# Kernel optimization log

Hardware: AMD Instinct MI355X
Metric: run time of the kernel (lower is better)

## Reference

```python
import jax, jax.numpy as jnp
import numpy as np

D_HEAD = 64
KV_GROUPS = 3
KSIZE = 7


def _win_idx(L, ksize):
    # NATTEN neighborhood: window centered at i, shifted to stay in-bounds.
    start = jnp.clip(jnp.arange(L) - ksize // 2, 0, L - ksize)  # [L]
    return start[:, None] + jnp.arange(ksize)[None, :]          # [L, k]


def _natten2d(q, k, v, ksize):
    # q,k,v: [n, nh, H, W, e]; q pre-scaled.
    H, W = q.shape[2], q.shape[3]
    ih = _win_idx(H, ksize)  # [H, k]
    iw = _win_idx(W, ksize)  # [W, k]
    # gather per-query key/value windows: [n, nh, H, W, k, k, e]
    kg = k[:, :, ih[:, None, :, None], iw[None, :, None, :], :]
    vg = v[:, :, ih[:, None, :, None], iw[None, :, None, :], :]
    logits = jnp.einsum('nhije,nhijabe->nhijab', q, kg)  # [n,nh,H,W,k,k]
    n_, nh = logits.shape[:2]
    a = jax.nn.softmax(logits.reshape(n_, nh, H, W, ksize * ksize), axis=-1)
    a = a.reshape(logits.shape)
    return jnp.einsum('nhijab,nhijabe->nhije', a, vg)  # [n,nh,H,W,e]


def _to_heads(p, nh, e):
    n, h, w, _ = p.shape
    return p.reshape(n, h, w, nh, e).transpose(0, 3, 1, 2, 4)  # [n,nh,h,w,e]


def setup_inputs() -> dict:
    key = jax.random.key(0)
    k1, k2, k3 = jax.random.split(key, 3)
    x = jax.random.normal(k1, (2, 32, 32, 768), dtype=jnp.float32)
    w_qkv = jax.random.normal(k2, (1280, 768), dtype=jnp.float32) * 0.02
    w_out = jax.random.normal(k3, (768, 768), dtype=jnp.float32) * 0.02
    return {"x": x, "w_qkv": w_qkv, "w_out": w_out}


def reference(x, w_qkv, w_out):
    n, H, W, d_model = x.shape
    q_heads = d_model // D_HEAD
    kv_heads = q_heads // KV_GROUPS
    qkv = x @ w_qkv.T  # [n,H,W,1280]
    q, k, v = jnp.split(
        qkv, [q_heads * D_HEAD, (q_heads + kv_heads) * D_HEAD], axis=-1)
    q = _to_heads(q, q_heads, D_HEAD)
    k = jnp.tile(_to_heads(k, kv_heads, D_HEAD), (1, KV_GROUPS, 1, 1, 1))
    v = jnp.tile(_to_heads(v, kv_heads, D_HEAD), (1, KV_GROUPS, 1, 1, 1))
    q = q / (D_HEAD ** 0.5)
    o = _natten2d(q, k, v, KSIZE)           # [n,nh,H,W,e]
    o = o.transpose(0, 2, 3, 1, 4).reshape(n, H, W, d_model)
    return o @ w_out.T
```

## Files before the change

### kernel.cpp

```cpp
#include <hip/hip_runtime.h>
#include <hip/hip_bf16.h>


typedef __attribute__((ext_vector_type(8))) __bf16 bf16x8;
typedef __attribute__((ext_vector_type(4))) float floatx4;
typedef unsigned short u16;

__device__ inline u16 f2bf(float f) {
    union { float f; unsigned u; } v; v.f = f;
    return (u16)((v.u + 0x7fff + ((v.u >> 16) & 1)) >> 16);
}

__device__ inline void gl_lds16(const void* g, void* l) {
    __builtin_amdgcn_global_load_lds(
        (const __attribute__((address_space(1))) void*)g,
        (__attribute__((address_space(3))) void*)l, 16, 0, 0);
}

__global__ __launch_bounds__(256) void convert_kernel(
    const float* __restrict__ x, const float* __restrict__ w1,
    const float* __restrict__ w2, u16* __restrict__ xb,
    u16* __restrict__ w1b, u16* __restrict__ w2b)
{
    int t = blockIdx.x * blockDim.x + threadIdx.x;
    const float* s; u16* d;
    if (t < 393216)      { s = x;  d = xb; }
    else if (t < 638976) { s = w1; d = w1b; t -= 393216; }
    else                 { s = w2; d = w2b; t -= 638976; }
    float4 v = ((const float4*)s)[t];
    ushort4 o;
    o.x = f2bf(v.x); o.y = f2bf(v.y); o.z = f2bf(v.z); o.w = f2bf(v.w);
    ((ushort4*)d)[t] = o;
}

template<int MODE>
__global__ __launch_bounds__(256) void gemm_nt(
    const u16* __restrict__ A, const u16* __restrict__ B,
    float* __restrict__ C, u16* __restrict__ Cb, u16* __restrict__ vT,
    int M, int N, int K)
{
    __shared__ __align__(16) u16 As[128 * 32];
    __shared__ __align__(16) u16 Bs[64 * 32];
    const int tid = threadIdx.x;
    const int lane = tid & 63;
    const int wave = tid >> 6;
    const int bm = blockIdx.y * 128;
    const int bn = blockIdx.x * 64;
    const int qr = (wave >> 1) * 64;
    const int qc = (wave & 1) * 32;

    floatx4 acc[4][2] = {};

    const int srA0 = wave * 32 + (lane >> 2);
    const int srA1 = srA0 + 16;
    const int srB  = wave * 16 + (lane >> 2);
    const int skel = (lane & 3) * 8;
    const u16* Ap0 = A + (size_t)(bm + srA0) * K + skel;
    const u16* Ap1 = A + (size_t)(bm + srA1) * K + skel;
    const u16* Bp  = B + (size_t)(bn + srB)  * K + skel;
    u16* AsC0 = &As[(wave * 2 + 0) * 512];
    u16* AsC1 = &As[(wave * 2 + 1) * 512];
    u16* BsC  = &Bs[wave * 512];

    const int fr = lane & 15;
    const int fk = (lane >> 4) * 8;

    for (int k0 = 0; k0 < K; k0 += 32) {
        gl_lds16(Ap0 + k0, AsC0);
        gl_lds16(Ap1 + k0, AsC1);
        gl_lds16(Bp  + k0, BsC);
        __syncthreads();
        bf16x8 af[4], bf[2];
        #pragma unroll
        for (int i = 0; i < 4; i++)
            af[i] = *(const bf16x8*)&As[(qr + i * 16 + fr) * 32 + fk];
        #pragma unroll
        for (int j = 0; j < 2; j++)
            bf[j] = *(const bf16x8*)&Bs[(qc + j * 16 + fr) * 32 + fk];
        #pragma unroll
        for (int i = 0; i < 4; i++)
            #pragma unroll
            for (int j = 0; j < 2; j++)
                acc[i][j] = __builtin_amdgcn_mfma_f32_16x16x32_bf16(
                    af[i], bf[j], acc[i][j], 0, 0, 0);
        __syncthreads();
    }

    const int cr = (lane >> 4) * 4;
    const int cc = lane & 15;
    #pragma unroll
    for (int i = 0; i < 4; i++) {
        #pragma unroll
        for (int j = 0; j < 2; j++) {
            const int row0 = bm + qr + i * 16 + cr;
            const int col  = bn + qc + j * 16 + cc;
            if (MODE == 0) {
                #pragma unroll
                for (int r = 0; r < 4; r++)
                    C[(size_t)(row0 + r) * N + col] = acc[i][j][r];
            } else {
                if (col < 1024) {
                    #pragma unroll
                    for (int r = 0; r < 4; r++)
                        Cb[(size_t)(row0 + r) * 1024 + col] = f2bf(acc[i][j][r]);
                } else {
                    ushort4 w;
                    w.x = f2bf(acc[i][j][0]); w.y = f2bf(acc[i][j][1]);
                    w.z = f2bf(acc[i][j][2]); w.w = f2bf(acc[i][j][3]);
                    *(ushort4*)&vT[(size_t)(col - 1024) * 2048 + row0] = w;
                }
            }
        }
    }
}

__global__ __launch_bounds__(256) void natten_mfma(
    const u16* __restrict__ qkv, const u16* __restrict__ vT,
    u16* __restrict__ o)
{
    __shared__ __align__(16) u16 Ks[224 * 72];
    __shared__ __align__(16) u16 Vs[64 * 224];
    __shared__ __align__(16) u16 Pw[4 * 512];
    const int h  = blockIdx.x;
    const int tb = blockIdx.y;
    const int g  = h & 3;
    const int batch = tb >> 4;
    const int ti = ((tb >> 2) & 3) * 8;
    const int tj = (tb & 3) * 8;
    const int wu_i = min(max(ti - 3, 0), 18);
    const int wu_j = min(max(tj - 3, 0), 18);
    const int tid = threadIdx.x, lane = tid & 63, wave = tid >> 6;
    const int pixbase = batch << 10;

    for (int c = tid; c < 1792; c += 256) {
        int n = c >> 3, seg = (c & 7) * 8;
        int a = n >> 4, b = min(n & 15, 13);
        int pix = pixbase + (wu_i + a) * 32 + wu_j + b;
        *(uint4*)&Ks[n * 72 + seg] =
            *(const uint4*)&qkv[(size_t)pix * 1024 + 768 + g * 64 + seg];
    }
    for (int c = tid; c < 14336; c += 256) {
        int d = c / 224, n = c % 224;
        int a = n >> 4, b = n & 15;
        u16 val = 0;
        if (b < 14) {
            int pix = pixbase + (wu_i + a) * 32 + wu_j + b;
            val = vT[(size_t)(g * 64 + d) * 2048 + pix];
        }
        Vs[d * 224 + n] = val;
    }
    __syncthreads();

    const int fr = lane & 15;
    const int fk = (lane >> 4) * 8;

    bf16x8 aq0, aq1;
    {
        int qq = wave * 16 + fr;
        int pixq = pixbase + (ti + (qq >> 3)) * 32 + tj + (qq & 7);
        const u16* qp = &qkv[(size_t)pixq * 1024 + h * 64];
        aq0 = *(const bf16x8*)(qp + fk);
        aq1 = *(const bf16x8*)(qp + 32 + fk);
    }

    bool colok[4]; int tlo[4], thi[4];
    #pragma unroll
    for (int r = 0; r < 4; r++) {
        int qq = wave * 16 + (lane >> 4) * 4 + r;
        int qi = ti + (qq >> 3), qj = tj + (qq & 7);
        int si = min(max(qi - 3, 0), 25);
        int sj = min(max(qj - 3, 0), 25);
        colok[r] = (fr < 14) && (wu_j + fr >= sj) && (wu_j + fr <= sj + 6);
        tlo[r] = si - wu_i; thi[r] = tlo[r] + 6;
    }

    float s[14][4];
    float mx[4] = {-1e30f, -1e30f, -1e30f, -1e30f};
    #pragma unroll
    for (int t = 0; t < 14; t++) {
        bf16x8 bk0 = *(const bf16x8*)&Ks[(t * 16 + fr) * 72 + fk];
        bf16x8 bk1 = *(const bf16x8*)&Ks[(t * 16 + fr) * 72 + 32 + fk];
        floatx4 a4 = {};
        a4 = __builtin_amdgcn_mfma_f32_16x16x32_bf16(aq0, bk0, a4, 0, 0, 0);
        a4 = __builtin_amdgcn_mfma_f32_16x16x32_bf16(aq1, bk1, a4, 0, 0, 0);
        #pragma unroll
        for (int r = 0; r < 4; r++) {
            bool v = colok[r] && (t >= tlo[r]) && (t <= thi[r]);
            s[t][r] = v ? a4[r] * 0.125f : -1e30f;
            mx[r] = fmaxf(mx[r], s[t][r]);
        }
    }
    #pragma unroll
    for (int r = 0; r < 4; r++) {
        mx[r] = fmaxf(mx[r], __shfl_xor(mx[r], 1));
        mx[r] = fmaxf(mx[r], __shfl_xor(mx[r], 2));
        mx[r] = fmaxf(mx[r], __shfl_xor(mx[r], 4));
        mx[r] = fmaxf(mx[r], __shfl_xor(mx[r], 8));
    }
    float l[4] = {0.f, 0.f, 0.f, 0.f};
    #pragma unroll
    for (int t = 0; t < 14; t++)
        #pragma unroll
        for (int r = 0; r < 4; r++) {
            float p = __expf(s[t][r] - mx[r]);
            s[t][r] = p; l[r] += p;
        }
    #pragma unroll
    for (int r = 0; r < 4; r++) {
        l[r] += __shfl_xor(l[r], 1);
        l[r] += __shfl_xor(l[r], 2);
        l[r] += __shfl_xor(l[r], 4);
        l[r] += __shfl_xor(l[r], 8);
    }
    float rinv[4];
    #pragma unroll
    for (int r = 0; r < 4; r++) rinv[r] = 1.0f / l[r];

    u16* pw = &Pw[wave * 512];
    floatx4 oacc[4] = {};
    #pragma unroll
    for (int kc = 0; kc < 7; kc++) {
        #pragma unroll
        for (int tt = 0; tt < 2; tt++) {
            int t = kc * 2 + tt;
            #pragma unroll
            for (int r = 0; r < 4; r++)
                pw[((lane >> 4) * 4 + r) * 32 + tt * 16 + fr] =
                    f2bf(s[t][r] * rinv[r]);
        }
        bf16x8 bp = *(const bf16x8*)&pw[fr * 32 + fk];
        #pragma unroll
        for (int u = 0; u < 4; u++) {
            bf16x8 av = *(const bf16x8*)&Vs[(u * 16 + fr) * 224 + kc * 32 + fk];
            oacc[u] = __builtin_amdgcn_mfma_f32_16x16x32_bf16(av, bp, oacc[u], 0, 0, 0);
        }
    }

    {
        int qq = wave * 16 + fr;
        int pixq = pixbase + (ti + (qq >> 3)) * 32 + tj + (qq & 7);
        u16* op = &o[(size_t)pixq * 768 + h * 64];
        #pragma unroll
        for (int u = 0; u < 4; u++) {
            ushort4 w;
            w.x = f2bf(oacc[u][0]); w.y = f2bf(oacc[u][1]);
            w.z = f2bf(oacc[u][2]); w.w = f2bf(oacc[u][3]);
            *(ushort4*)(op + u * 16 + (lane >> 4) * 4) = w;
        }
    }
}

extern "C" void kernel_launch(void* const* d_in, const int* in_sizes, int n_in,
                              void* d_out, int out_size, void* d_ws, size_t ws_size,
                              hipStream_t stream)
{
    const float* x     = (const float*)d_in[0];
    const float* w_qkv = (const float*)d_in[1];
    const float* w_out = (const float*)d_in[2];
    float* out = (float*)d_out;

    char* ws = (char*)d_ws;
    u16* qkvb = (u16*)ws; ws += (size_t)2048 * 1024 * 2;
    u16* vTb  = (u16*)ws; ws += (size_t)256 * 2048 * 2 + 64;
    u16* xb   = (u16*)ws; ws += (size_t)2048 * 768 * 2;
    u16* w1b  = (u16*)ws; ws += (size_t)1280 * 768 * 2;
    u16* w2b  = (u16*)ws; ws += (size_t)768 * 768 * 2;
    u16* ob   = (u16*)ws;

    convert_kernel<<<dim3(3072), dim3(256), 0, stream>>>(x, w_qkv, w_out, xb, w1b, w2b);

    gemm_nt<1><<<dim3(1280 / 64, 2048 / 128), dim3(256), 0, stream>>>(
        xb, w1b, nullptr, qkvb, vTb, 2048, 1280, 768);

    natten_mfma<<<dim3(12, 32), dim3(256), 0, stream>>>(qkvb, vTb, ob);

    gemm_nt<0><<<dim3(768 / 64, 2048 / 128), dim3(256), 0, stream>>>(
        ob, w2b, out, nullptr, nullptr, 2048, 768, 768);
}
```

Measured before the change: 123.1 us.

## Use 64x64 GEMM tiles with 128-deep K stages and restructure V tile load

The GEMM tile shrinks from 128x64 to 64x64, doubling the grid size. Each stage now loads 128 K-elements via eight direct-to-LDS loads per wave, so there are fewer barriers per K and more MFMAs per sync. The NATTEN V-transpose staging loop replaces per-element division and modulo with a wave-per-16-rows layout using precomputed offsets. The aim is better occupancy on small GEMMs and fewer loop-overhead and index costs, at the price of less operand reuse per tile and larger LDS use.

```diff
diff --git a/kernel.cpp b/kernel.cpp
--- a/kernel.cpp
+++ b/kernel.cpp
@@ -39,61 +39,63 @@
     float* __restrict__ C, u16* __restrict__ Cb, u16* __restrict__ vT,
     int M, int N, int K)
 {
-    __shared__ __align__(16) u16 As[128 * 32];
-    __shared__ __align__(16) u16 Bs[64 * 32];
+    __shared__ __align__(16) u16 As[4 * 64 * 32];
+    __shared__ __align__(16) u16 Bs[4 * 64 * 32];
     const int tid = threadIdx.x;
     const int lane = tid & 63;
     const int wave = tid >> 6;
-    const int bm = blockIdx.y * 128;
+    const int bm = blockIdx.y * 64;
     const int bn = blockIdx.x * 64;
-    const int qr = (wave >> 1) * 64;
+    const int qr = (wave >> 1) * 32;
     const int qc = (wave & 1) * 32;
 
-    floatx4 acc[4][2] = {};
-
-    const int srA0 = wave * 32 + (lane >> 2);
-    const int srA1 = srA0 + 16;
-    const int srB  = wave * 16 + (lane >> 2);
-    const int skel = (lane & 3) * 8;
-    const u16* Ap0 = A + (size_t)(bm + srA0) * K + skel;
-    const u16* Ap1 = A + (size_t)(bm + srA1) * K + skel;
-    const u16* Bp  = B + (size_t)(bn + srB)  * K + skel;
-    u16* AsC0 = &As[(wave * 2 + 0) * 512];
-    u16* AsC1 = &As[(wave * 2 + 1) * 512];
-    u16* BsC  = &Bs[wave * 512];
+    floatx4 acc[2][2] = {};
+
+    const u16* Xsrc = (wave < 2) ? A : B;
+    const int   bx  = (wave < 2) ? bm : bn;
+    u16* Xlds       = (wave < 2) ? As : Bs;
+    const int half  = wave & 1;
+    const int l2 = lane >> 2;
+    const int l3 = (lane & 3) * 8;
+    const u16* gptr[8];
+    u16* lptr[8];
+    #pragma unroll
+    for (int cc = 0; cc < 8; cc++) {
+        int c = half * 8 + cc, kc = c & 3, rg = c >> 2;
+        gptr[cc] = Xsrc + (size_t)(bx + rg * 16 + l2) * K + kc * 32 + l3;
+        lptr[cc] = Xlds + kc * 2048 + rg * 512;
+    }
 
     const int fr = lane & 15;
     const int fk = (lane >> 4) * 8;
 
-    for (int k0 = 0; k0 < K; k0 += 32) {
-        gl_lds16(Ap0 + k0, AsC0);
-        gl_lds16(Ap1 + k0, AsC1);
-        gl_lds16(Bp  + k0, BsC);
+    for (int k0 = 0; k0 < K; k0 += 128) {
+        #pragma unroll
+        for (int cc = 0; cc < 8; cc++)
+            gl_lds16(gptr[cc] + k0, lptr[cc]);
         __syncthreads();
-        bf16x8 af[4], bf[2];
-        #pragma unroll
-        for (int i = 0; i < 4; i++)
-            af[i] = *(const bf16x8*)&As[(qr + i * 16 + fr) * 32 + fk];
-        #pragma unroll
-        for (int j = 0; j < 2; j++)
-            bf[j] = *(const bf16x8*)&Bs[(qc + j * 16 + fr) * 32 + fk];
-        #pragma unroll
-        for (int i = 0; i < 4; i++)
-            #pragma unroll
-            for (int j = 0; j < 2; j++)
-                acc[i][j] = __builtin_amdgcn_mfma_f32_16x16x32_bf16(
-                    af[i], bf[j], acc[i][j], 0, 0, 0);
+        #pragma unroll
+        for (int kc = 0; kc < 4; kc++) {
+            bf16x8 af0 = *(const bf16x8*)&As[kc * 2048 + (qr +      fr) * 32 + fk];
+            bf16x8 af1 = *(const bf16x8*)&As[kc * 2048 + (qr + 16 + fr) * 32 + fk];
+            bf16x8 bf0 = *(const bf16x8*)&Bs[kc * 2048 + (qc +      fr) * 32 + fk];
+            bf16x8 bf1 = *(const bf16x8*)&Bs[kc * 2048 + (qc + 16 + fr) * 32 + fk];
+            acc[0][0] = __builtin_amdgcn_mfma_f32_16x16x32_bf16(af0, bf0, acc[0][0], 0, 0, 0);
+            acc[0][1] = __builtin_amdgcn_mfma_f32_16x16x32_bf16(af0, bf1, acc[0][1], 0, 0, 0);
+            acc[1][0] = __builtin_amdgcn_mfma_f32_16x16x32_bf16(af1, bf0, acc[1][0], 0, 0, 0);
+            acc[1][1] = __builtin_amdgcn_mfma_f32_16x16x32_bf16(af1, bf1, acc[1][1], 0, 0, 0);
+        }
         __syncthreads();
     }
 
     const int cr = (lane >> 4) * 4;
-    const int cc = lane & 15;
-    #pragma unroll
-    for (int i = 0; i < 4; i++) {
+    const int ccol = lane & 15;
+    #pragma unroll
+    for (int i = 0; i < 2; i++) {
         #pragma unroll
         for (int j = 0; j < 2; j++) {
             const int row0 = bm + qr + i * 16 + cr;
-            const int col  = bn + qc + j * 16 + cc;
+            const int col  = bn + qc + j * 16 + ccol;
             if (MODE == 0) {
                 #pragma unroll
                 for (int r = 0; r < 4; r++)
@@ -139,15 +141,28 @@
         *(uint4*)&Ks[n * 72 + seg] =
             *(const uint4*)&qkv[(size_t)pix * 1024 + 768 + g * 64 + seg];
     }
-    for (int c = tid; c < 14336; c += 256) {
-        int d = c / 224, n = c % 224;
-        int a = n >> 4, b = n & 15;
-        u16 val = 0;
-        if (b < 14) {
-            int pix = pixbase + (wu_i + a) * 32 + wu_j + b;
-            val = vT[(size_t)(g * 64 + d) * 2048 + pix];
-        }
-        Vs[d * 224 + n] = val;
+    {
+        const int b  = lane & 15;
+        const int ar = lane >> 4;
+        bool vok[4]; int voff[4];
+        #pragma unroll
+        for (int rr = 0; rr < 4; rr++) {
+            int a = ar + rr * 4;
+            vok[rr]  = (a < 14) && (b < 14);
+            voff[rr] = (wu_i + a) * 32 + wu_j + b;
+        }
+        const u16* vsrc = &vT[(size_t)(g * 64 + wave * 16) * 2048 + pixbase];
+        #pragma unroll 4
+        for (int dd = 0; dd < 16; dd++) {
+            #pragma unroll
+            for (int rr = 0; rr < 4; rr++) {
+                int a = ar + rr * 4;
+                if (a < 14)
+                    Vs[(wave * 16 + dd) * 224 + rr * 64 + lane] =
+                        vok[rr] ? vsrc[voff[rr]] : (u16)0;
+            }
+            vsrc += 2048;
+        }
     }
     __syncthreads();
 
@@ -269,11 +284,11 @@
 
     convert_kernel<<<dim3(3072), dim3(256), 0, stream>>>(x, w_qkv, w_out, xb, w1b, w2b);
 
-    gemm_nt<1><<<dim3(1280 / 64, 2048 / 128), dim3(256), 0, stream>>>(
+    gemm_nt<1><<<dim3(1280 / 64, 2048 / 64), dim3(256), 0, stream>>>(
         xb, w1b, nullptr, qkvb, vTb, 2048, 1280, 768);
 
     natten_mfma<<<dim3(12, 32), dim3(256), 0, stream>>>(qkvb, vTb, ob);
 
-    gemm_nt<0><<<dim3(768 / 64, 2048 / 128), dim3(256), 0, stream>>>(
+    gemm_nt<0><<<dim3(768 / 64, 2048 / 64), dim3(256), 0, stream>>>(
         ob, w2b, out, nullptr, nullptr, 2048, 768, 768);
 }
```

New measurement: 108.7 us. 1.13x faster.
